# Kernel optimization log

Hardware: AMD Instinct MI355X
Metric: run time of the kernel (lower is better)

Reference implementation:

```python
import jax, jax.numpy as jnp
import numpy as np

LN_EPS = 1e-5  # torch nn.LayerNorm default


def _layernorm(h):
    # elementwise_affine=False LayerNorm over last dim
    mu = jnp.mean(h, axis=-1, keepdims=True)
    var = jnp.var(h, axis=-1, keepdims=True)
    return (h - mu) * jax.lax.rsqrt(var + LN_EPS)


def setup_inputs() -> dict:
    key = jax.random.key(0)
    ks = jax.random.split(key, 7)
    B, M, D, L = 10240, 8, 512, 3  # b=1024*10 and m=8 are hardcoded in the module
    rn = lambda k, shape, scale=1.0: jax.random.normal(k, shape, dtype=jnp.float32) * scale
    return {
        "x":   rn(ks[0], (B, D)),
        "Ws":  rn(ks[1], (L, M, D, D), 0.05),  # per-layer basis weight tensors (m,i,j)
        "bs":  rn(ks[2], (L, M, D), 0.05),     # per-layer basis biases (m,i)
        "pWs": rn(ks[3], (L, B, M)),           # per-sample weight-mixing coeffs
        "pbs": rn(ks[4], (L, B, M)),           # per-sample bias-mixing coeffs
        "gWs": rn(ks[5], (L, B, D, 1)),        # gates (squeezed in forward)
        "gbs": rn(ks[6], (L, B, D)),
    }


def reference(x, Ws, bs, pWs, pbs, gWs, gbs):
    L = Ws.shape[0]
    for l in range(L):
        gW = gWs[l][..., 0]                                  # (b, i)
        # 'bi,bm,mij,bj->bi' without materializing (b,i,j):
        y = jnp.einsum('mij,bj->bmi', Ws[l], x)              # (b, m, i)
        Wx = gW * jnp.einsum('bm,bmi->bi', pWs[l], y)        # (b, i)
        # 'bj,bm,mj->bj' (bias lives in output dim)
        bias = gbs[l] * jnp.einsum('bm,mi->bi', pbs[l], bs[l])
        h = Wx + bias
        if l != L - 1:  # hidden layers: LayerNorm (no affine) + ELU; last: identity
            h = jax.nn.elu(_layernorm(h))
        x = h
    return x
```

## Files before the change

### kernel.cpp

```cpp
#include <hip/hip_runtime.h>
#include <math.h>

#define BB   10240
#define DD   512
#define MM   8

typedef _Float16 h8 __attribute__((ext_vector_type(8)));
typedef float    f4 __attribute__((ext_vector_type(4)));

__device__ __forceinline__ void gload16(const void* g, void* l) {
    __builtin_amdgcn_global_load_lds(
        (__attribute__((address_space(1))) void*)(g),
        (__attribute__((address_space(3))) void*)(l), 16, 0, 0);
}

__global__ void __launch_bounds__(256) cvt_f32_f16(const float* __restrict__ s,
                                                   _Float16* __restrict__ d, int n8) {
    int i = blockIdx.x * 256 + threadIdx.x;
    if (i >= n8) return;
    const float4* sp = (const float4*)s + (size_t)i * 2;
    float4 a = sp[0], b = sp[1];
    h8 o = { (_Float16)a.x, (_Float16)a.y, (_Float16)a.z, (_Float16)a.w,
             (_Float16)b.x, (_Float16)b.y, (_Float16)b.z, (_Float16)b.w };
    *(h8*)(d + (size_t)i * 8) = o;
}

template <int HALF_OUT>
__global__ void __launch_bounds__(128, 2) gemm_layer(
    const _Float16* __restrict__ xh,
    const _Float16* __restrict__ Wh,
    const float*  __restrict__ pW,
    const float*  __restrict__ pb,
    const float*  __restrict__ bsv,
    const float*  __restrict__ gW,
    const float*  __restrict__ gb,
    float* __restrict__ outf,
    _Float16* __restrict__ outh)
{
    __shared__ __align__(16) _Float16 Wl[2][3][32 * 64];

    const int tid  = threadIdx.x;
    const int lane = tid & 63;
    const int w    = tid >> 6;
    const int ln16 = lane & 15, quad = lane >> 4;
    const int bn0  = blockIdx.x * 64;
    const int bm0  = blockIdx.y * 128;

    _Float16 pwh[8][8];
    #pragma unroll
    for (int mt = 0; mt < 8; ++mt) {
        const float* pp = pW + (size_t)(bm0 + mt * 16 + ln16) * MM;
        float4 p0 = *(const float4*)pp;
        float4 p1 = *(const float4*)(pp + 4);
        pwh[mt][0] = (_Float16)p0.x; pwh[mt][1] = (_Float16)p0.y;
        pwh[mt][2] = (_Float16)p0.z; pwh[mt][3] = (_Float16)p0.w;
        pwh[mt][4] = (_Float16)p1.x; pwh[mt][5] = (_Float16)p1.y;
        pwh[mt][6] = (_Float16)p1.z; pwh[mt][7] = (_Float16)p1.w;
    }

    const _Float16* ab0 = xh + (size_t)(bm0 + ln16) * DD + quad * 8;

    f4 acc[8][2] = {};
    h8 afr[2][8];

#define STW(S_, M_, JC_) do {                                                  \
    _Pragma("unroll")                                                          \
    for (int c = 0; c < 4; ++c) {                                              \
        int rit     = c * 8 + (lane >> 3);             \
        int logical = (lane & 7) ^ (lane >> 3);           \
        const _Float16* gp = Wh + (size_t)(M_) * (DD * DD)                     \
                               + (size_t)(bn0 + w * 32 + rit) * DD             \
                               + (JC_) * 64 + logical * 8;                     \
        gload16(gp, &Wl[w][S_][c * 512]);                                      \
    }                                                                          \
} while (0)

#define AL(JC) do {                                                            \
    _Pragma("unroll")                                                          \
    for (int _ks = 0; _ks < 2; ++_ks)                                          \
        _Pragma("unroll")                                                      \
        for (int _mt = 0; _mt < 8; ++_mt)                                      \
            afr[_ks][_mt] = *(const h8*)(ab0 + (size_t)_mt * (16 * DD)         \
                                         + (size_t)(JC) * 64 + _ks * 32);      \
} while (0)

#define GS(T_, N_, PA_) do {                                                   \
    if ((T_) + 2 <= 63) STW((((T_) + 2) % 3), (((T_) + 2) & 7),                \
                            (((T_) + 2) >> 3));                                \
    asm volatile("s_waitcnt vmcnt(%0)" :: "i"(N_) : "memory");                 \
    __builtin_amdgcn_sched_barrier(0);                                         \
    h8 wfr[2][2];                                                              \
    _Pragma("unroll")                                                          \
    for (int ks = 0; ks < 2; ++ks)                                             \
        _Pragma("unroll")                                                      \
        for (int nt = 0; nt < 2; ++nt) {                                       \
            int row  = nt * 16 + ln16;                                         \
            int phys = (ks * 4 + quad) ^ (ln16 & 7);                           \
            wfr[ks][nt] = *(const h8*)&Wl[w][(T_) % 3][row * 64 + phys * 8];   \
        }                                                                      \
    _Pragma("unroll")                                                          \
    for (int ks = 0; ks < 2; ++ks)                                             \
        _Pragma("unroll")                                                      \
        for (int mt = 0; mt < 8; ++mt) {                                       \
            h8 as = afr[ks][mt] * pwh[mt][(T_) & 7];      \
            acc[mt][0] = __builtin_amdgcn_mfma_f32_16x16x32_f16(               \
                as, wfr[ks][0], acc[mt][0], 0, 0, 0);                          \
            acc[mt][1] = __builtin_amdgcn_mfma_f32_16x16x32_f16(               \
                as, wfr[ks][1], acc[mt][1], 0, 0, 0);                          \
        }                                                                      \
    if (PA_) AL(((T_) >> 3) + 1);                                              \
} while (0)

    AL(0);
    STW(0, 0, 0);
    STW(1, 1, 0);

    GS( 0,  8, 0); GS( 1,  8, 0); GS( 2,  8, 0); GS( 3,  8, 0);
    GS( 4,  8, 0); GS( 5,  8, 0); GS( 6,  8, 0); GS( 7,  8, 1);
    GS( 8, 24, 0); GS( 9,  8, 0); GS(10,  8, 0); GS(11,  8, 0);
    GS(12,  8, 0); GS(13,  8, 0); GS(14,  8, 0); GS(15,  8, 1);
    GS(16, 24, 0); GS(17,  8, 0); GS(18,  8, 0); GS(19,  8, 0);
    GS(20,  8, 0); GS(21,  8, 0); GS(22,  8, 0); GS(23,  8, 1);
    GS(24, 24, 0); GS(25,  8, 0); GS(26,  8, 0); GS(27,  8, 0);
    GS(28,  8, 0); GS(29,  8, 0); GS(30,  8, 0); GS(31,  8, 1);
    GS(32, 24, 0); GS(33,  8, 0); GS(34,  8, 0); GS(35,  8, 0);
    GS(36,  8, 0); GS(37,  8, 0); GS(38,  8, 0); GS(39,  8, 1);
    GS(40, 24, 0); GS(41,  8, 0); GS(42,  8, 0); GS(43,  8, 0);
    GS(44,  8, 0); GS(45,  8, 0); GS(46,  8, 0); GS(47,  8, 1);
    GS(48, 24, 0); GS(49,  8, 0); GS(50,  8, 0); GS(51,  8, 0);
    GS(52,  8, 0); GS(53,  8, 0); GS(54,  8, 0); GS(55,  8, 1);
    GS(56, 24, 0); GS(57,  8, 0); GS(58,  8, 0); GS(59,  8, 0);
    GS(60,  8, 0); GS(61,  8, 0); GS(62,  4, 0); GS(63,  0, 0);

#undef GS
#undef AL
#undef STW

    const int i0 = bn0 + w * 32 + ln16;
    const int i1 = i0 + 16;
    float bs0[8], bs1[8];
    #pragma unroll
    for (int m2 = 0; m2 < 8; ++m2) {
        bs0[m2] = bsv[m2 * DD + i0];
        bs1[m2] = bsv[m2 * DD + i1];
    }
    #pragma unroll
    for (int mt = 0; mt < 8; ++mt) {
        #pragma unroll
        for (int r = 0; r < 4; ++r) {
            int b = bm0 + mt * 16 + quad * 4 + r;
            float4 p0 = *(const float4*)(pb + (size_t)b * MM);
            float4 p1 = *(const float4*)(pb + (size_t)b * MM + 4);
            float bias0 = p0.x*bs0[0] + p0.y*bs0[1] + p0.z*bs0[2] + p0.w*bs0[3]
                        + p1.x*bs0[4] + p1.y*bs0[5] + p1.z*bs0[6] + p1.w*bs0[7];
            float bias1 = p0.x*bs1[0] + p0.y*bs1[1] + p0.z*bs1[2] + p0.w*bs1[3]
                        + p1.x*bs1[4] + p1.y*bs1[5] + p1.z*bs1[6] + p1.w*bs1[7];
            float v0 = gW[(size_t)b * DD + i0] * acc[mt][0][r] + gb[(size_t)b * DD + i0] * bias0;
            float v1 = gW[(size_t)b * DD + i1] * acc[mt][1][r] + gb[(size_t)b * DD + i1] * bias1;
            if (HALF_OUT) {
                outh[(size_t)b * DD + i0] = (_Float16)v0;
                outh[(size_t)b * DD + i1] = (_Float16)v1;
            } else {
                outf[(size_t)b * DD + i0] = v0;
                outf[(size_t)b * DD + i1] = v1;
            }
        }
    }
}

__global__ void __launch_bounds__(256) ln_elu_h(const _Float16* __restrict__ h,
                                                _Float16* __restrict__ xo) {
    const int w    = threadIdx.x >> 6;
    const int lane = threadIdx.x & 63;
    const int row  = blockIdx.x * 4 + w;
    h8 v = *(const h8*)(h + (size_t)row * DD + lane * 8);
    float f[8], s = 0.f, q = 0.f;
    #pragma unroll
    for (int i = 0; i < 8; ++i) { f[i] = (float)v[i]; s += f[i]; q += f[i] * f[i]; }
    #pragma unroll
    for (int off = 1; off < 64; off <<= 1) {
        s += __shfl_xor(s, off);
        q += __shfl_xor(q, off);
    }
    float mu   = s * (1.0f / 512.0f);
    float var  = q * (1.0f / 512.0f) - mu * mu;
    float rstd = rsqrtf(var + 1e-5f);
    h8 o;
    #pragma unroll
    for (int i = 0; i < 8; ++i) {
        float t = (f[i] - mu) * rstd;
        t = t > 0.0f ? t : expm1f(t);
        o[i] = (_Float16)t;
    }
    *(h8*)(xo + (size_t)row * DD + lane * 8) = o;
}

extern "C" void kernel_launch(void* const* d_in, const int* in_sizes, int n_in,
                              void* d_out, int out_size, void* d_ws, size_t ws_size,
                              hipStream_t stream) {
    const float* x   = (const float*)d_in[0];
    const float* Ws  = (const float*)d_in[1];
    const float* bs  = (const float*)d_in[2];
    const float* pWs = (const float*)d_in[3];
    const float* pbs = (const float*)d_in[4];
    const float* gWs = (const float*)d_in[5];
    const float* gbs = (const float*)d_in[6];
    float* out = (float*)d_out;

    _Float16* Wh = (_Float16*)d_ws;
    _Float16* xh = Wh + (size_t)3 * MM * DD * DD;
    _Float16* hh = xh + (size_t)BB * DD;

    const int wsl = MM * DD * DD;
    const int bsl = MM * DD;
    const int pl  = BB * MM;
    const int gl  = BB * DD;

    cvt_f32_f16<<<3072, 256, 0, stream>>>(Ws, Wh, 786432);
    cvt_f32_f16<<<2560, 256, 0, stream>>>(x, xh, 655360);

    dim3 gg(DD / 64, BB / 128);

    gemm_layer<1><<<gg, 128, 0, stream>>>(xh, Wh, pWs, pbs, bs, gWs, gbs,
                                          nullptr, hh);
    ln_elu_h<<<BB / 4, 256, 0, stream>>>(hh, xh);
    gemm_layer<1><<<gg, 128, 0, stream>>>(xh, Wh + wsl, pWs + pl, pbs + pl,
                                          bs + bsl, gWs + gl, gbs + gl,
                                          nullptr, hh);
    ln_elu_h<<<BB / 4, 256, 0, stream>>>(hh, xh);
    gemm_layer<0><<<gg, 128, 0, stream>>>(xh, Wh + 2 * wsl, pWs + 2 * pl,
                                          pbs + 2 * pl, bs + 2 * bsl,
                                          gWs + 2 * gl, gbs + 2 * gl,
                                          out, nullptr);
}
```

Before: 374.5 us.

## Stage activation tiles through LDS with async global-to-LDS loads and barriers

Activation fragments were loaded straight from global memory into registers, with each wave re-reading the same rows. They are now staged cooperatively into a shared 128x64 LDS buffer using async global_load_lds with an XOR swizzle, then read into registers. The pipeline schedule gains block-wide barriers and adjusted vmcnt waits so the single A buffer is refilled safely between K-chunks. This cuts redundant global traffic and register-side load latency, at the cost of extra barriers, more LDS use (which may reduce occupancy), and a single-buffered A tile that can stall.

After: 361.2 us. 1.04x faster.

```diff
diff --git a/kernel.cpp b/kernel.cpp
--- a/kernel.cpp
+++ b/kernel.cpp
@@ -38,6 +38,7 @@
     _Float16* __restrict__ outh)
 {
     __shared__ __align__(16) _Float16 Wl[2][3][32 * 64];
+    __shared__ __align__(16) _Float16 Ab[128 * 64];
 
     const int tid  = threadIdx.x;
     const int lane = tid & 63;
@@ -58,16 +59,14 @@
         pwh[mt][6] = (_Float16)p1.z; pwh[mt][7] = (_Float16)p1.w;
     }
 
-    const _Float16* ab0 = xh + (size_t)(bm0 + ln16) * DD + quad * 8;
-
     f4 acc[8][2] = {};
     h8 afr[2][8];
 
 #define STW(S_, M_, JC_) do {                                                  \
     _Pragma("unroll")                                                          \
     for (int c = 0; c < 4; ++c) {                                              \
-        int rit     = c * 8 + (lane >> 3);             \
-        int logical = (lane & 7) ^ (lane >> 3);           \
+        int rit     = c * 8 + (lane >> 3);                                     \
+        int logical = (lane & 7) ^ (lane >> 3);                                \
         const _Float16* gp = Wh + (size_t)(M_) * (DD * DD)                     \
                                + (size_t)(bn0 + w * 32 + rit) * DD             \
                                + (JC_) * 64 + logical * 8;                     \
@@ -75,20 +74,34 @@
     }                                                                          \
 } while (0)
 
-#define AL(JC) do {                                                            \
+#define STA(JC_) do {                                                          \
+    _Pragma("unroll")                                                          \
+    for (int c = 0; c < 8; ++c) {                                              \
+        int rit     = w * 64 + c * 8 + (lane >> 3);                            \
+        int logical = (lane & 7) ^ (lane >> 3);                                \
+        const _Float16* gp = xh + (size_t)(bm0 + rit) * DD                     \
+                                + (JC_) * 64 + logical * 8;                    \
+        gload16(gp, &Ab[rit * 64]);                                            \
+    }                                                                          \
+} while (0)
+
+#define AFR() do {                                                             \
     _Pragma("unroll")                                                          \
     for (int _ks = 0; _ks < 2; ++_ks)                                          \
         _Pragma("unroll")                                                      \
-        for (int _mt = 0; _mt < 8; ++_mt)                                      \
-            afr[_ks][_mt] = *(const h8*)(ab0 + (size_t)_mt * (16 * DD)         \
-                                         + (size_t)(JC) * 64 + _ks * 32);      \
+        for (int _mt = 0; _mt < 8; ++_mt) {                                    \
+            int _phys = (_ks * 4 + quad) ^ (ln16 & 7);                         \
+            afr[_ks][_mt] = *(const h8*)&Ab[(_mt * 16 + ln16) * 64             \
+                                            + _phys * 8];                      \
+        }                                                                      \
 } while (0)
 
-#define GS(T_, N_, PA_) do {                                                   \
+#define GS(T_, N_, AF_, SA_, B1_, B2_) do {                                    \
     if ((T_) + 2 <= 63) STW((((T_) + 2) % 3), (((T_) + 2) & 7),                \
                             (((T_) + 2) >> 3));                                \
     asm volatile("s_waitcnt vmcnt(%0)" :: "i"(N_) : "memory");                 \
     __builtin_amdgcn_sched_barrier(0);                                         \
+    if (AF_) AFR();                                                            \
     h8 wfr[2][2];                                                              \
     _Pragma("unroll")                                                          \
     for (int ks = 0; ks < 2; ++ks)                                             \
@@ -108,32 +121,90 @@
             acc[mt][1] = __builtin_amdgcn_mfma_f32_16x16x32_f16(               \
                 as, wfr[ks][1], acc[mt][1], 0, 0, 0);                          \
         }                                                                      \
-    if (PA_) AL(((T_) >> 3) + 1);                                              \
+    if (SA_) STA(((T_) >> 3) + 1);                                             \
+    if (B2_) { asm volatile("s_waitcnt lgkmcnt(0)" ::: "memory");              \
+               __builtin_amdgcn_s_barrier();                                   \
+               asm volatile("" ::: "memory"); }                                \
+    if (B1_) { __builtin_amdgcn_s_barrier();                                   \
+               asm volatile("" ::: "memory"); }                                \
 } while (0)
 
-    AL(0);
+    STA(0);
     STW(0, 0, 0);
     STW(1, 1, 0);
-
-    GS( 0,  8, 0); GS( 1,  8, 0); GS( 2,  8, 0); GS( 3,  8, 0);
-    GS( 4,  8, 0); GS( 5,  8, 0); GS( 6,  8, 0); GS( 7,  8, 1);
-    GS( 8, 24, 0); GS( 9,  8, 0); GS(10,  8, 0); GS(11,  8, 0);
-    GS(12,  8, 0); GS(13,  8, 0); GS(14,  8, 0); GS(15,  8, 1);
-    GS(16, 24, 0); GS(17,  8, 0); GS(18,  8, 0); GS(19,  8, 0);
-    GS(20,  8, 0); GS(21,  8, 0); GS(22,  8, 0); GS(23,  8, 1);
-    GS(24, 24, 0); GS(25,  8, 0); GS(26,  8, 0); GS(27,  8, 0);
-    GS(28,  8, 0); GS(29,  8, 0); GS(30,  8, 0); GS(31,  8, 1);
-    GS(32, 24, 0); GS(33,  8, 0); GS(34,  8, 0); GS(35,  8, 0);
-    GS(36,  8, 0); GS(37,  8, 0); GS(38,  8, 0); GS(39,  8, 1);
-    GS(40, 24, 0); GS(41,  8, 0); GS(42,  8, 0); GS(43,  8, 0);
-    GS(44,  8, 0); GS(45,  8, 0); GS(46,  8, 0); GS(47,  8, 1);
-    GS(48, 24, 0); GS(49,  8, 0); GS(50,  8, 0); GS(51,  8, 0);
-    GS(52,  8, 0); GS(53,  8, 0); GS(54,  8, 0); GS(55,  8, 1);
-    GS(56, 24, 0); GS(57,  8, 0); GS(58,  8, 0); GS(59,  8, 0);
-    GS(60,  8, 0); GS(61,  8, 0); GS(62,  4, 0); GS(63,  0, 0);
+    asm volatile("s_waitcnt vmcnt(8)" ::: "memory");
+    __builtin_amdgcn_sched_barrier(0);
+    __builtin_amdgcn_s_barrier();
+    asm volatile("" ::: "memory");
+
+    GS(  0,  8, 1, 0, 0, 1);
+    GS(  1,  8, 0, 0, 0, 0);
+    GS(  2,  8, 0, 1, 0, 0);
+    GS(  3, 16, 0, 0, 0, 0);
+    GS(  4, 16, 0, 0, 0, 0);
+    GS(  5,  8, 0, 0, 0, 0);
+    GS(  6,  8, 0, 0, 0, 0);
+    GS(  7,  8, 0, 0, 1, 0);
+    GS(  8,  8, 1, 0, 0, 1);
+    GS(  9,  8, 0, 0, 0, 0);
+    GS( 10,  8, 0, 1, 0, 0);
+    GS( 11, 16, 0, 0, 0, 0);
+    GS( 12, 16, 0, 0, 0, 0);
+    GS( 13,  8, 0, 0, 0, 0);
+    GS( 14,  8, 0, 0, 0, 0);
+    GS( 15,  8, 0, 0, 1, 0);
+    GS( 16,  8, 1, 0, 0, 1);
+    GS( 17,  8, 0, 0, 0, 0);
+    GS( 18,  8, 0, 1, 0, 0);
+    GS( 19, 16, 0, 0, 0, 0);
+    GS( 20, 16, 0, 0, 0, 0);
+    GS( 21,  8, 0, 0, 0, 0);
+    GS( 22,  8, 0, 0, 0, 0);
+    GS( 23,  8, 0, 0, 1, 0);
+    GS( 24,  8, 1, 0, 0, 1);
+    GS( 25,  8, 0, 0, 0, 0);
+    GS( 26,  8, 0, 1, 0, 0);
+    GS( 27, 16, 0, 0, 0, 0);
+    GS( 28, 16, 0, 0, 0, 0);
+    GS( 29,  8, 0, 0, 0, 0);
+    GS( 30,  8, 0, 0, 0, 0);
+    GS( 31,  8, 0, 0, 1, 0);
+    GS( 32,  8, 1, 0, 0, 1);
+    GS( 33,  8, 0, 0, 0, 0);
+    GS( 34,  8, 0, 1, 0, 0);
+    GS( 35, 16, 0, 0, 0, 0);
+    GS( 36, 16, 0, 0, 0, 0);
+    GS( 37,  8, 0, 0, 0, 0);
+    GS( 38,  8, 0, 0, 0, 0);
+    GS( 39,  8, 0, 0, 1, 0);
+    GS( 40,  8, 1, 0, 0, 1);
+    GS( 41,  8, 0, 0, 0, 0);
+    GS( 42,  8, 0, 1, 0, 0);
+    GS( 43, 16, 0, 0, 0, 0);
+    GS( 44, 16, 0, 0, 0, 0);
+    GS( 45,  8, 0, 0, 0, 0);
+    GS( 46,  8, 0, 0, 0, 0);
+    GS( 47,  8, 0, 0, 1, 0);
+    GS( 48,  8, 1, 0, 0, 1);
+    GS( 49,  8, 0, 0, 0, 0);
+    GS( 50,  8, 0, 1, 0, 0);
+    GS( 51, 16, 0, 0, 0, 0);
+    GS( 52, 16, 0, 0, 0, 0);
+    GS( 53,  8, 0, 0, 0, 0);
+    GS( 54,  8, 0, 0, 0, 0);
+    GS( 55,  8, 0, 0, 1, 0);
+    GS( 56,  8, 1, 0, 0, 0);
+    GS( 57,  8, 0, 0, 0, 0);
+    GS( 58,  8, 0, 0, 0, 0);
+    GS( 59,  8, 0, 0, 0, 0);
+    GS( 60,  8, 0, 0, 0, 0);
+    GS( 61,  8, 0, 0, 0, 0);
+    GS( 62,  4, 0, 0, 0, 0);
+    GS( 63,  0, 0, 0, 0, 0);
 
 #undef GS
-#undef AL
+#undef AFR
+#undef STA
 #undef STW
 
     const int i0 = bn0 + w * 32 + ln16;
```
